# Kernel tuning notes

Measured on AMD Instinct MI355X. Metric: run time of the kernel, lower is better.

Reference implementation:

```python
import math
import jax, jax.numpy as jnp
import numpy as np

CHUNK_LEN = 64
NUM_HEADS = 16
HIDDEN = 1024
HEAD = HIDDEN // NUM_HEADS


def setup_inputs() -> dict:
    key = jax.random.key(0)
    ks = jax.random.split(key, 8)
    B, S, C, N, L = 4, 2048, 32, 2, 128
    scale = 1.0 / math.sqrt(HIDDEN)
    return {
        "query": jax.random.normal(ks[0], (B, S, HIDDEN), jnp.float32),
        "kv": jax.random.normal(ks[1], (B, C, N, L, HIDDEN), jnp.float32),
        "Wq": jax.random.normal(ks[2], (HIDDEN, HIDDEN), jnp.float32) * scale,
        "bq": jnp.zeros((HIDDEN,), jnp.float32),
        "Wk": jax.random.normal(ks[3], (HIDDEN, HIDDEN), jnp.float32) * scale,
        "bk": jnp.zeros((HIDDEN,), jnp.float32),
        "Wv": jax.random.normal(ks[4], (HIDDEN, HIDDEN), jnp.float32) * scale,
        "bv": jnp.zeros((HIDDEN,), jnp.float32),
    }


def reference(query, kv, Wq, bq, Wk, bk, Wv, bv):
    B, S, H = query.shape
    _, C, N, L, _ = kv.shape
    # shift query right by chunk_len-1 and pad to n_chunks*chunk_len
    q = query[:, CHUNK_LEN - 1:]
    add_len = C * CHUNK_LEN - q.shape[1]
    q = jnp.pad(q, ((0, 0), (0, add_len), (0, 0)))
    q = q.reshape(B, C, CHUNK_LEN, H)
    q = (q @ Wq.T + bq).reshape(B, C, CHUNK_LEN, NUM_HEADS, HEAD)
    k = (kv @ Wk.T + bk).reshape(B, C, N, L, NUM_HEADS, HEAD)
    v = (kv @ Wv.T + bv).reshape(B, C, N, L, NUM_HEADS, HEAD)
    # scores: [B, C, heads, chunk_len, N, L]
    attn = jnp.einsum("bcihd,bcnjhd->bchinj", q, k) / math.sqrt(HEAD)
    # softmax over flattened neighbor dims (n, j)
    attn = jax.nn.softmax(attn.reshape(B, C, NUM_HEADS, CHUNK_LEN, N * L), axis=-1)
    attn = attn.reshape(B, C, NUM_HEADS, CHUNK_LEN, N, L)
    h = jnp.einsum("bchinj,bcnjhd->bcihd", attn, v).reshape(B, C * CHUNK_LEN, H)
    # shift left: prepend chunk_len-1 zeros, truncate to seq_len
    h = jnp.pad(h, ((0, 0), (CHUNK_LEN - 1, 0), (0, 0)))[:, :S]
    return h
```

## Files before the change

kernel.cpp:

```cpp
#include <hip/hip_runtime.h>
#include <stdint.h>

#define HD 1024
#define SEQ 2048
#define NC 32

typedef __bf16 bf16x4 __attribute__((ext_vector_type(4)));
typedef __bf16 bf16x8 __attribute__((ext_vector_type(8)));
typedef float f32x4 __attribute__((ext_vector_type(4)));

__device__ inline unsigned short f2bf(float f) {
  union { float f; unsigned int u; } v; v.f = f;
  unsigned int r = v.u + 0x7fffu + ((v.u >> 16) & 1u);
  return (unsigned short)(r >> 16);
}
__device__ inline unsigned int pk2bf(float a, float b) {
  return (unsigned int)f2bf(a) | ((unsigned int)f2bf(b) << 16);
}
__device__ inline bf16x8 ld_frag8(const unsigned short* p) {
  bf16x4 lo = *(const bf16x4*)p;
  bf16x4 hi = *(const bf16x4*)(p + 4);
  return __builtin_shufflevector(lo, hi, 0, 1, 2, 3, 4, 5, 6, 7);
}
__device__ inline void glds16(const unsigned short* g, unsigned short* l) {
  __builtin_amdgcn_global_load_lds(
      (const __attribute__((address_space(1))) unsigned int*)g,
      (__attribute__((address_space(3))) unsigned int*)l, 16, 0, 0);
}

__global__ __launch_bounds__(256) void zero_head_kernel(float* __restrict__ out) {
  int i = (blockIdx.x * 256 + threadIdx.x) * 4;
  int b = i / 64512;
  int r = i - b * 64512;
  *(float4*)(out + (size_t)b * (SEQ * HD) + r) = make_float4(0.f, 0.f, 0.f, 0.f);
}

__global__ __launch_bounds__(256) void cvt_kernel(const float* __restrict__ in,
                                                  unsigned short* __restrict__ out, int n8) {
  int i = blockIdx.x * 256 + threadIdx.x;
  if (i < n8) {
    float4 a = ((const float4*)in)[(size_t)i * 2];
    float4 b = ((const float4*)in)[(size_t)i * 2 + 1];
    ((uint4*)out)[i] = make_uint4(pk2bf(a.x, a.y), pk2bf(a.z, a.w),
                                  pk2bf(b.x, b.y), pk2bf(b.z, b.w));
  }
}

__global__ __launch_bounds__(256) void cvt_q_kernel(const float* __restrict__ q,
                                                    unsigned short* __restrict__ out) {
  int i = blockIdx.x * 256 + threadIdx.x;
  int g = i >> 7, c8 = (i & 127) * 8;
  int b = g >> 11, tt = g & 2047;
  uint4 o = make_uint4(0, 0, 0, 0);
  if (tt < 1985) {
    const float* src = q + ((size_t)(b << 11) + tt + 63) * HD + c8;
    float4 a = *(const float4*)src;
    float4 bb = *(const float4*)(src + 4);
    o = make_uint4(pk2bf(a.x, a.y), pk2bf(a.z, a.w), pk2bf(bb.x, bb.y), pk2bf(bb.z, bb.w));
  }
  *(uint4*)(out + (size_t)g * HD + c8) = o;
}

__global__ __launch_bounds__(256, 2) void gemm_bf_kernel(
    const unsigned short* __restrict__ A, const unsigned short* __restrict__ W,
    const float* __restrict__ bias, unsigned short* __restrict__ Cout, int store_vt) {
  __shared__ unsigned short lds_a[128 * 32];
  __shared__ unsigned short lds_b[128 * 32];
  const int t = threadIdx.x;
  const int l = t & 63, w = t >> 6;
  const int wm = w >> 1, wn = w & 1;
  const int lr = l & 15, lq = l >> 4;
  const size_t arow0 = (size_t)blockIdx.y * 128;
  const size_t brow0 = (size_t)blockIdx.x * 128;
  const int c0 = t, c1 = 256 + t;
  const unsigned short* a0 = A + (arow0 + (c0 >> 2)) * HD + (c0 & 3) * 8;
  const unsigned short* a1 = A + (arow0 + (c1 >> 2)) * HD + (c1 & 3) * 8;
  const unsigned short* b0 = W + (brow0 + (c0 >> 2)) * HD + (c0 & 3) * 8;
  const unsigned short* b1 = W + (brow0 + (c1 >> 2)) * HD + (c1 & 3) * 8;

  f32x4 acc[4][4];
  for (int i = 0; i < 4; i++)
    for (int j = 0; j < 4; j++) acc[i][j] = (f32x4){0.f, 0.f, 0.f, 0.f};

  for (int kk = 0; kk < 32; ++kk) {
    const int k0 = kk * 32;
    __syncthreads();
    glds16(a0 + k0, lds_a + c0 * 8);
    glds16(a1 + k0, lds_a + c1 * 8);
    glds16(b0 + k0, lds_b + c0 * 8);
    glds16(b1 + k0, lds_b + c1 * 8);
    __syncthreads();
    bf16x8 af[4], bfr[4];
    for (int mt = 0; mt < 4; ++mt)
      af[mt] = *(const bf16x8*)(lds_a + (wm * 64 + mt * 16 + lr) * 32 + lq * 8);
    for (int nt = 0; nt < 4; ++nt)
      bfr[nt] = *(const bf16x8*)(lds_b + (wn * 64 + nt * 16 + lr) * 32 + lq * 8);
    for (int mt = 0; mt < 4; ++mt)
      for (int nt = 0; nt < 4; ++nt)
        acc[mt][nt] = __builtin_amdgcn_mfma_f32_16x16x32_bf16(af[mt], bfr[nt], acc[mt][nt], 0, 0, 0);
  }

  if (!store_vt) {
    for (int nt = 0; nt < 4; ++nt) {
      int n = blockIdx.x * 128 + wn * 64 + nt * 16 + lr;
      float bvv = bias[n];
      for (int mt = 0; mt < 4; ++mt) {
        size_t mbase = arow0 + wm * 64 + mt * 16 + lq * 4;
        for (int r = 0; r < 4; ++r)
          Cout[(mbase + r) * HD + n] = f2bf(acc[mt][nt][r] + bvv);
      }
    }
  } else {
    for (int nt = 0; nt < 4; ++nt) {
      int n = blockIdx.x * 128 + wn * 64 + nt * 16 + lr;
      float bvv = bias[n];
      int h = n >> 6, d = n & 63;
      for (int mt = 0; mt < 4; ++mt) {
        size_t m0 = arow0 + wm * 64 + mt * 16 + lq * 4;
        size_t bc = m0 >> 8, j = m0 & 255;
        *(ushort4*)(Cout + ((bc * 16 + h) * 64 + d) * 256 + j) =
            make_ushort4(f2bf(acc[mt][nt][0] + bvv), f2bf(acc[mt][nt][1] + bvv),
                         f2bf(acc[mt][nt][2] + bvv), f2bf(acc[mt][nt][3] + bvv));
      }
    }
  }
}

__global__ __launch_bounds__(256, 2) void gemm_f32_kernel(
    const float* __restrict__ A, const float* __restrict__ W,
    const float* __restrict__ bias, unsigned short* __restrict__ Cout,
    int store_vt, int qremap) {
  __shared__ unsigned short lds_a[128 * 32];
  __shared__ unsigned short lds_b[128 * 32];
  const int t = threadIdx.x;
  const int l = t & 63, w = t >> 6;
  const int wm = w >> 1, wn = w & 1;
  const int lr = l & 15, lq = l >> 4;
  const size_t arow0 = (size_t)blockIdx.y * 128;
  const size_t brow0 = (size_t)blockIdx.x * 128;

  f32x4 acc[4][4];
  for (int i = 0; i < 4; i++)
    for (int j = 0; j < 4; j++) acc[i][j] = (f32x4){0.f, 0.f, 0.f, 0.f};

  for (int kk = 0; kk < 32; ++kk) {
    const int k0 = kk * 32;
    uint4 av[2], bv[2];
    for (int p = 0; p < 2; ++p) {
      int chunk = p * 256 + t;
      int row = chunk >> 2, c8 = (chunk & 3) * 8;
      size_t grow = arow0 + row;
      bool valid = true;
      const float* srcA;
      if (qremap) {
        int bb = (int)(grow >> 11), tt = (int)(grow & 2047);
        valid = tt < 1985;
        srcA = A + ((size_t)(bb << 11) + tt + 63) * HD + k0 + c8;
      } else {
        srcA = A + grow * HD + k0 + c8;
      }
      if (valid) {
        float4 x = *(const float4*)srcA, y = *(const float4*)(srcA + 4);
        av[p] = make_uint4(pk2bf(x.x, x.y), pk2bf(x.z, x.w), pk2bf(y.x, y.y), pk2bf(y.z, y.w));
      } else av[p] = make_uint4(0, 0, 0, 0);
      const float* srcB = W + (brow0 + row) * HD + k0 + c8;
      float4 x = *(const float4*)srcB, y = *(const float4*)(srcB + 4);
      bv[p] = make_uint4(pk2bf(x.x, x.y), pk2bf(x.z, x.w), pk2bf(y.x, y.y), pk2bf(y.z, y.w));
    }
    __syncthreads();
    for (int p = 0; p < 2; ++p) {
      int chunk = p * 256 + t;
      *(uint4*)(lds_a + chunk * 8) = av[p];
      *(uint4*)(lds_b + chunk * 8) = bv[p];
    }
    __syncthreads();
    bf16x8 af[4], bfr[4];
    for (int mt = 0; mt < 4; ++mt)
      af[mt] = *(const bf16x8*)(lds_a + (wm * 64 + mt * 16 + lr) * 32 + lq * 8);
    for (int nt = 0; nt < 4; ++nt)
      bfr[nt] = *(const bf16x8*)(lds_b + (wn * 64 + nt * 16 + lr) * 32 + lq * 8);
    for (int mt = 0; mt < 4; ++mt)
      for (int nt = 0; nt < 4; ++nt)
        acc[mt][nt] = __builtin_amdgcn_mfma_f32_16x16x32_bf16(af[mt], bfr[nt], acc[mt][nt], 0, 0, 0);
  }

  if (!store_vt) {
    for (int nt = 0; nt < 4; ++nt) {
      int n = blockIdx.x * 128 + wn * 64 + nt * 16 + lr;
      float bvv = bias[n];
      for (int mt = 0; mt < 4; ++mt) {
        size_t mbase = arow0 + wm * 64 + mt * 16 + lq * 4;
        for (int r = 0; r < 4; ++r)
          Cout[(mbase + r) * HD + n] = f2bf(acc[mt][nt][r] + bvv);
      }
    }
  } else {
    for (int nt = 0; nt < 4; ++nt) {
      int n = blockIdx.x * 128 + wn * 64 + nt * 16 + lr;
      float bvv = bias[n];
      int h = n >> 6, d = n & 63;
      for (int mt = 0; mt < 4; ++mt) {
        size_t m0 = arow0 + wm * 64 + mt * 16 + lq * 4;
        size_t bc = m0 >> 8, j = m0 & 255;
        *(ushort4*)(Cout + ((bc * 16 + h) * 64 + d) * 256 + j) =
            make_ushort4(f2bf(acc[mt][nt][0] + bvv), f2bf(acc[mt][nt][1] + bvv),
                         f2bf(acc[mt][nt][2] + bvv), f2bf(acc[mt][nt][3] + bvv));
      }
    }
  }
}

#define QK_STRIDE 68
#define P_STRIDE 260

__global__ __launch_bounds__(256, 3) void attn_kernel(
    const unsigned short* __restrict__ Qp, const unsigned short* __restrict__ Kp,
    const unsigned short* __restrict__ Vt, float* __restrict__ out) {
  __shared__ unsigned short q_s[64 * QK_STRIDE];
  __shared__ unsigned short k_s[256 * QK_STRIDE];
  const int t = threadIdx.x;
  const int l = t & 63, w = t >> 6;
  const int lr = l & 15, lq = l >> 4;
  const int bid = blockIdx.x;
  const int head = bid & 15, cc = (bid >> 4) & 31, b = bid >> 9;
  const size_t qrow0 = (size_t)(b * NC + cc) * 64;
  const size_t kvrow0 = (size_t)(b * NC + cc) * 256;
  const int hcol = head * 64;
  const unsigned short* vbase = Vt + ((size_t)((b * NC + cc) * 16 + head) * 64) * 256;

  for (int p = 0; p < 4; ++p) {
    int chunk = p * 256 + t;
    int row = chunk >> 4, c4 = (chunk & 15) * 4;
    *(uint2*)(q_s + row * QK_STRIDE + c4) = *(const uint2*)(Qp + (qrow0 + row) * HD + hcol + c4);
  }
  for (int p = 0; p < 16; ++p) {
    int chunk = p * 256 + t;
    int row = chunk >> 4, c4 = (chunk & 15) * 4;
    *(uint2*)(k_s + row * QK_STRIDE + c4) = *(const uint2*)(Kp + (kvrow0 + row) * HD + hcol + c4);
  }
  __syncthreads();

  bf16x8 qa0 = ld_frag8(q_s + (w * 16 + lr) * QK_STRIDE + lq * 8);
  bf16x8 qa1 = ld_frag8(q_s + (w * 16 + lr) * QK_STRIDE + 32 + lq * 8);
  f32x4 sc[16];
  for (int nt = 0; nt < 16; ++nt) {
    bf16x8 kb0 = ld_frag8(k_s + (nt * 16 + lr) * QK_STRIDE + lq * 8);
    bf16x8 kb1 = ld_frag8(k_s + (nt * 16 + lr) * QK_STRIDE + 32 + lq * 8);
    f32x4 a = (f32x4){0.f, 0.f, 0.f, 0.f};
    a = __builtin_amdgcn_mfma_f32_16x16x32_bf16(qa0, kb0, a, 0, 0, 0);
    a = __builtin_amdgcn_mfma_f32_16x16x32_bf16(qa1, kb1, a, 0, 0, 0);
    sc[nt] = a;
  }
  float mrow[4] = {-1e30f, -1e30f, -1e30f, -1e30f};
  for (int nt = 0; nt < 16; ++nt)
    for (int r = 0; r < 4; ++r) mrow[r] = fmaxf(mrow[r], sc[nt][r]);
  for (int off = 1; off < 16; off <<= 1)
    for (int r = 0; r < 4; ++r) mrow[r] = fmaxf(mrow[r], __shfl_xor(mrow[r], off, 16));
  float srow[4] = {0.f, 0.f, 0.f, 0.f};
  const float cexp = 0.18033688011112042f;
  for (int nt = 0; nt < 16; ++nt)
    for (int r = 0; r < 4; ++r) {
      float p = exp2f((sc[nt][r] - mrow[r]) * cexp);
      sc[nt][r] = p;
      srow[r] += p;
    }
  for (int off = 1; off < 16; off <<= 1)
    for (int r = 0; r < 4; ++r) srow[r] += __shfl_xor(srow[r], off, 16);

  __syncthreads();

  for (int nt = 0; nt < 16; ++nt)
    for (int r = 0; r < 4; ++r)
      k_s[(w * 16 + lq * 4 + r) * P_STRIDE + nt * 16 + lr] = f2bf(sc[nt][r]);

  f32x4 o[4];
  for (int i = 0; i < 4; ++i) o[i] = (f32x4){0.f, 0.f, 0.f, 0.f};
  for (int ks = 0; ks < 8; ++ks) {
    bf16x8 pa = ld_frag8(k_s + (w * 16 + lr) * P_STRIDE + ks * 32 + lq * 8);
    for (int nt2 = 0; nt2 < 4; ++nt2) {
      bf16x8 vb = *(const bf16x8*)(vbase + (size_t)(nt2 * 16 + lr) * 256 + ks * 32 + lq * 8);
      o[nt2] = __builtin_amdgcn_mfma_f32_16x16x32_bf16(pa, vb, o[nt2], 0, 0, 0);
    }
  }

  for (int r = 0; r < 4; ++r) {
    int strip = w * 16 + lq * 4 + r;
    int trow = cc * 64 + strip;
    if (trow < 1985) {
      size_t orow = (size_t)b * SEQ + trow + 63;
      float inv = 1.0f / srow[r];
      for (int nt2 = 0; nt2 < 4; ++nt2)
        out[orow * HD + hcol + nt2 * 16 + lr] = o[nt2][r] * inv;
    }
  }
}

extern "C" void kernel_launch(void* const* d_in, const int* in_sizes, int n_in,
                              void* d_out, int out_size, void* d_ws, size_t ws_size,
                              hipStream_t stream) {
  (void)in_sizes; (void)n_in; (void)out_size;
  const float* query = (const float*)d_in[0];
  const float* kv    = (const float*)d_in[1];
  const float* Wq    = (const float*)d_in[2];
  const float* bq    = (const float*)d_in[3];
  const float* Wk    = (const float*)d_in[4];
  const float* bk    = (const float*)d_in[5];
  const float* Wv    = (const float*)d_in[6];
  const float* bv    = (const float*)d_in[7];
  float* out = (float*)d_out;

  unsigned short* Qp  = (unsigned short*)d_ws;
  unsigned short* Kp  = Qp + (size_t)8192 * 1024;
  unsigned short* Vt  = Kp + (size_t)32768 * 1024;
  unsigned short* Qbf = Vt + (size_t)32768 * 1024;
  unsigned short* KVb = Qbf + (size_t)8192 * 1024;
  unsigned short* Wqb = KVb + (size_t)32768 * 1024;
  unsigned short* Wkb = Wqb + (size_t)1024 * 1024;
  unsigned short* Wvb = Wkb + (size_t)1024 * 1024;
  const size_t need = ((size_t)8192 * 1024 * 2 + (size_t)32768 * 1024 * 2 + (size_t)1024 * 1024 * 3) * 2;
  const bool big = ws_size >= need;

  zero_head_kernel<<<dim3(252), dim3(256), 0, stream>>>(out);
  if (big) {
    cvt_q_kernel<<<dim3(4096), dim3(256), 0, stream>>>(query, Qbf);
    cvt_kernel<<<dim3(16384), dim3(256), 0, stream>>>(kv, KVb, 4194304);
    cvt_kernel<<<dim3(512), dim3(256), 0, stream>>>(Wq, Wqb, 131072);
    cvt_kernel<<<dim3(512), dim3(256), 0, stream>>>(Wk, Wkb, 131072);
    cvt_kernel<<<dim3(512), dim3(256), 0, stream>>>(Wv, Wvb, 131072);
    gemm_bf_kernel<<<dim3(8, 64), dim3(256), 0, stream>>>(Qbf, Wqb, bq, Qp, 0);
    gemm_bf_kernel<<<dim3(8, 256), dim3(256), 0, stream>>>(KVb, Wkb, bk, Kp, 0);
    gemm_bf_kernel<<<dim3(8, 256), dim3(256), 0, stream>>>(KVb, Wvb, bv, Vt, 1);
  } else {
    gemm_f32_kernel<<<dim3(8, 64), dim3(256), 0, stream>>>(query, Wq, bq, Qp, 0, 1);
    gemm_f32_kernel<<<dim3(8, 256), dim3(256), 0, stream>>>(kv, Wk, bk, Kp, 0, 0);
    gemm_f32_kernel<<<dim3(8, 256), dim3(256), 0, stream>>>(kv, Wv, bv, Vt, 1, 0);
  }
  attn_kernel<<<dim3(2048), dim3(256), 0, stream>>>(Qp, Kp, Vt, out);
}
```

Measured before the change: 519.6 us.

## Fuse K and V projection GEMMs sharing A tiles, add block swizzle

```diff
diff --git a/kernel.cpp b/kernel.cpp
--- a/kernel.cpp
+++ b/kernel.cpp
@@ -26,6 +26,11 @@
   __builtin_amdgcn_global_load_lds(
       (const __attribute__((address_space(1))) unsigned int*)g,
       (__attribute__((address_space(3))) unsigned int*)l, 16, 0, 0);
+}
+__device__ inline int2 swz_bid() {
+  int lin = blockIdx.y * 8 + blockIdx.x;
+  int s = (lin & 7) * (int)gridDim.y + (lin >> 3);
+  return make_int2(s & 7, s >> 3);
 }
 
 __global__ __launch_bounds__(256) void zero_head_kernel(float* __restrict__ out) {
@@ -70,8 +75,9 @@
   const int l = t & 63, w = t >> 6;
   const int wm = w >> 1, wn = w & 1;
   const int lr = l & 15, lq = l >> 4;
-  const size_t arow0 = (size_t)blockIdx.y * 128;
-  const size_t brow0 = (size_t)blockIdx.x * 128;
+  const int2 bid = swz_bid();
+  const size_t arow0 = (size_t)bid.y * 128;
+  const size_t brow0 = (size_t)bid.x * 128;
   const int c0 = t, c1 = 256 + t;
   const unsigned short* a0 = A + (arow0 + (c0 >> 2)) * HD + (c0 & 3) * 8;
   const unsigned short* a1 = A + (arow0 + (c1 >> 2)) * HD + (c1 & 3) * 8;
@@ -102,7 +108,7 @@
 
   if (!store_vt) {
     for (int nt = 0; nt < 4; ++nt) {
-      int n = blockIdx.x * 128 + wn * 64 + nt * 16 + lr;
+      int n = bid.x * 128 + wn * 64 + nt * 16 + lr;
       float bvv = bias[n];
       for (int mt = 0; mt < 4; ++mt) {
         size_t mbase = arow0 + wm * 64 + mt * 16 + lq * 4;
@@ -112,7 +118,7 @@
     }
   } else {
     for (int nt = 0; nt < 4; ++nt) {
-      int n = blockIdx.x * 128 + wn * 64 + nt * 16 + lr;
+      int n = bid.x * 128 + wn * 64 + nt * 16 + lr;
       float bvv = bias[n];
       int h = n >> 6, d = n & 63;
       for (int mt = 0; mt < 4; ++mt) {
@@ -122,6 +128,90 @@
             make_ushort4(f2bf(acc[mt][nt][0] + bvv), f2bf(acc[mt][nt][1] + bvv),
                          f2bf(acc[mt][nt][2] + bvv), f2bf(acc[mt][nt][3] + bvv));
       }
+    }
+  }
+}
+
+__global__ __launch_bounds__(256, 2) void gemm_kv_kernel(
+    const unsigned short* __restrict__ A, const unsigned short* __restrict__ Wk,
+    const unsigned short* __restrict__ Wv, const float* __restrict__ bk,
+    const float* __restrict__ bv, unsigned short* __restrict__ Kout,
+    unsigned short* __restrict__ Vt) {
+  __shared__ unsigned short lds_a[128 * 32];
+  __shared__ unsigned short lds_k[128 * 32];
+  __shared__ unsigned short lds_v[128 * 32];
+  const int t = threadIdx.x;
+  const int l = t & 63, w = t >> 6;
+  const int wm = w >> 1, wn = w & 1;
+  const int lr = l & 15, lq = l >> 4;
+  const int2 bid = swz_bid();
+  const size_t arow0 = (size_t)bid.y * 128;
+  const size_t brow0 = (size_t)bid.x * 128;
+  const int c0 = t, c1 = 256 + t;
+  const unsigned short* a0 = A + (arow0 + (c0 >> 2)) * HD + (c0 & 3) * 8;
+  const unsigned short* a1 = A + (arow0 + (c1 >> 2)) * HD + (c1 & 3) * 8;
+  const unsigned short* k0p = Wk + (brow0 + (c0 >> 2)) * HD + (c0 & 3) * 8;
+  const unsigned short* k1p = Wk + (brow0 + (c1 >> 2)) * HD + (c1 & 3) * 8;
+  const unsigned short* v0p = Wv + (brow0 + (c0 >> 2)) * HD + (c0 & 3) * 8;
+  const unsigned short* v1p = Wv + (brow0 + (c1 >> 2)) * HD + (c1 & 3) * 8;
+
+  f32x4 acck[4][4], accv[4][4];
+  for (int i = 0; i < 4; i++)
+    for (int j = 0; j < 4; j++) {
+      acck[i][j] = (f32x4){0.f, 0.f, 0.f, 0.f};
+      accv[i][j] = (f32x4){0.f, 0.f, 0.f, 0.f};
+    }
+
+  for (int kk = 0; kk < 32; ++kk) {
+    const int k0 = kk * 32;
+    __syncthreads();
+    glds16(a0 + k0, lds_a + c0 * 8);
+    glds16(a1 + k0, lds_a + c1 * 8);
+    glds16(k0p + k0, lds_k + c0 * 8);
+    glds16(k1p + k0, lds_k + c1 * 8);
+    glds16(v0p + k0, lds_v + c0 * 8);
+    glds16(v1p + k0, lds_v + c1 * 8);
+    __syncthreads();
+    bf16x8 af[4];
+    for (int mt = 0; mt < 4; ++mt)
+      af[mt] = *(const bf16x8*)(lds_a + (wm * 64 + mt * 16 + lr) * 32 + lq * 8);
+    {
+      bf16x8 bfr[4];
+      for (int nt = 0; nt < 4; ++nt)
+        bfr[nt] = *(const bf16x8*)(lds_k + (wn * 64 + nt * 16 + lr) * 32 + lq * 8);
+      for (int mt = 0; mt < 4; ++mt)
+        for (int nt = 0; nt < 4; ++nt)
+          acck[mt][nt] = __builtin_amdgcn_mfma_f32_16x16x32_bf16(af[mt], bfr[nt], acck[mt][nt], 0, 0, 0);
+    }
+    {
+      bf16x8 bfr[4];
+      for (int nt = 0; nt < 4; ++nt)
+        bfr[nt] = *(const bf16x8*)(lds_v + (wn * 64 + nt * 16 + lr) * 32 + lq * 8);
+      for (int mt = 0; mt < 4; ++mt)
+        for (int nt = 0; nt < 4; ++nt)
+          accv[mt][nt] = __builtin_amdgcn_mfma_f32_16x16x32_bf16(af[mt], bfr[nt], accv[mt][nt], 0, 0, 0);
+    }
+  }
+
+  for (int nt = 0; nt < 4; ++nt) {
+    int n = bid.x * 128 + wn * 64 + nt * 16 + lr;
+    float bvv = bk[n];
+    for (int mt = 0; mt < 4; ++mt) {
+      size_t mbase = arow0 + wm * 64 + mt * 16 + lq * 4;
+      for (int r = 0; r < 4; ++r)
+        Kout[(mbase + r) * HD + n] = f2bf(acck[mt][nt][r] + bvv);
+    }
+  }
+  for (int nt = 0; nt < 4; ++nt) {
+    int n = bid.x * 128 + wn * 64 + nt * 16 + lr;
+    float bvv = bv[n];
+    int h = n >> 6, d = n & 63;
+    for (int mt = 0; mt < 4; ++mt) {
+      size_t m0 = arow0 + wm * 64 + mt * 16 + lq * 4;
+      size_t bc = m0 >> 8, j = m0 & 255;
+      *(ushort4*)(Vt + ((bc * 16 + h) * 64 + d) * 256 + j) =
+          make_ushort4(f2bf(accv[mt][nt][0] + bvv), f2bf(accv[mt][nt][1] + bvv),
+                       f2bf(accv[mt][nt][2] + bvv), f2bf(accv[mt][nt][3] + bvv));
     }
   }
 }
@@ -328,8 +418,7 @@
     cvt_kernel<<<dim3(512), dim3(256), 0, stream>>>(Wk, Wkb, 131072);
     cvt_kernel<<<dim3(512), dim3(256), 0, stream>>>(Wv, Wvb, 131072);
     gemm_bf_kernel<<<dim3(8, 64), dim3(256), 0, stream>>>(Qbf, Wqb, bq, Qp, 0);
-    gemm_bf_kernel<<<dim3(8, 256), dim3(256), 0, stream>>>(KVb, Wkb, bk, Kp, 0);
-    gemm_bf_kernel<<<dim3(8, 256), dim3(256), 0, stream>>>(KVb, Wvb, bv, Vt, 1);
+    gemm_kv_kernel<<<dim3(8, 256), dim3(256), 0, stream>>>(KVb, Wkb, Wvb, bk, bv, Kp, Vt);
   } else {
     gemm_f32_kernel<<<dim3(8, 64), dim3(256), 0, stream>>>(query, Wq, bq, Qp, 0, 1);
     gemm_f32_kernel<<<dim3(8, 256), dim3(256), 0, stream>>>(kv, Wk, bk, Kp, 0, 0);
```

Result: faster. 484.4 us (-6.8%).
